# Kernel tuning notes

Measured on AMD Instinct MI355X. Metric: run time of the kernel, lower is better.

## Reference

```python
import jax, jax.numpy as jnp
import numpy as np

B, H, W, C = 16, 64, 64, 256
NH = 8          # num_heads
WS = 8          # window size (8,8) from shift=2
HID = 1024      # mlp hidden = 4*C
EPS = 1e-5


def _rel_index():
    # relative_position_index exactly as in the torch module (meshgrid 'ij')
    ch = np.arange(WS)
    coords = np.stack(np.meshgrid(ch, ch, indexing='ij'))          # (2, WS, WS)
    flat = coords.reshape(2, -1)                                    # (2, N)
    rel = flat[:, :, None] - flat[:, None, :]                       # (2, N, N)
    rel = rel.transpose(1, 2, 0).astype(np.int64)                   # (N, N, 2)
    rel[..., 0] += WS - 1
    rel[..., 1] += WS - 1
    rel[..., 0] *= 2 * WS - 1
    return jnp.asarray(rel.sum(-1))                                 # (N, N)


def _ln(x, w, b):
    m = x.mean(-1, keepdims=True)
    v = jnp.mean((x - m) ** 2, axis=-1, keepdims=True)
    return (x - m) / jnp.sqrt(v + EPS) * w + b


def setup_inputs() -> dict:
    key = jax.random.key(0)
    ks = jax.random.split(key, 16)
    std = 0.02
    n_bias = (2 * WS - 1) * (2 * WS - 1)  # 225
    return {
        'x': jax.random.normal(ks[0], (B, H * W, C), jnp.float32),
        'norm1_w': jnp.ones((C,), jnp.float32),
        'norm1_b': jnp.zeros((C,), jnp.float32),
        'qkv_w': jax.random.normal(ks[1], (3 * C, C), jnp.float32) * std,
        'qkv_b': jnp.zeros((3 * C,), jnp.float32),
        'rel_bias': jax.random.normal(ks[2], (n_bias, NH), jnp.float32) * std,
        'proj_w': jax.random.normal(ks[3], (C, C), jnp.float32) * std,
        'proj_b': jnp.zeros((C,), jnp.float32),
        'norm2_w': jnp.ones((C,), jnp.float32),
        'norm2_b': jnp.zeros((C,), jnp.float32),
        'fc1_w': jax.random.normal(ks[4], (HID, C), jnp.float32) * std,
        'fc1_b': jnp.zeros((HID,), jnp.float32),
        'dw_w': jax.random.normal(ks[5], (3, 3, 1, HID), jnp.float32) * std,  # HWIO depthwise
        'dw_b': jnp.zeros((HID,), jnp.float32),
        'fc2_w': jax.random.normal(ks[6], (C, HID), jnp.float32) * std,
        'fc2_b': jnp.zeros((C,), jnp.float32),
    }


def reference(x, norm1_w, norm1_b, qkv_w, qkv_b, rel_bias, proj_w, proj_b,
              norm2_w, norm2_b, fc1_w, fc1_b, dw_w, dw_b, fc2_w, fc2_b):
    S = (H // WS) * (W // WS)   # num windows = 64
    N = WS * WS                 # tokens per window = 64
    shortcut = x
    h = _ln(x, norm1_w, norm1_b).reshape(B, H, W, C)
    # window partition -> (B, S, N, C), then permute to (B, N, S, C)
    hw = (h.reshape(B, H // WS, WS, W // WS, WS, C)
            .transpose(0, 1, 3, 2, 4, 5)
            .reshape(B, S, N, C))
    xw = hw.transpose(0, 2, 1, 3)            # (B, N, S, C)
    # qkv over flattened (N*S) tokens; heads split the S*C feature dim
    xf = xw.reshape(B, N * S, C)
    qkv = xf @ qkv_w.T + qkv_b               # (B, N*S, 3C)
    qkv = qkv.reshape(B, N, 3, NH, S * C // NH).transpose(2, 0, 3, 1, 4)
    q, k, v = qkv[0], qkv[1], qkv[2]         # (B, NH, N, S*C/NH)
    scale = (C // NH) ** -0.5
    attn = jnp.einsum('bhnd,bhmd->bhnm', q, k) * scale   # (B, NH, N, N)
    idx = _rel_index()
    bias = rel_bias[idx.reshape(-1)].reshape(N, N, NH).transpose(2, 0, 1)
    attn = jax.nn.softmax(attn + bias[None], axis=-1)
    out = jnp.einsum('bhnm,bhmd->bhnd', attn, v)         # (B, NH, N, S*C/NH)
    out = out.transpose(0, 2, 1, 3).reshape(B, N * S, C)
    out = (out @ proj_w.T + proj_b).reshape(B, N, S, C).transpose(0, 2, 1, 3)  # (B,S,N,C)
    # window reverse -> (B, H*W, C)
    xr = (out.reshape(B, H // WS, W // WS, WS, WS, C)
             .transpose(0, 1, 3, 2, 4, 5)
             .reshape(B, H * W, C))
    x = shortcut + xr
    # conv-based MLP (eval mode, dropout = identity)
    y = _ln(x, norm2_w, norm2_b).reshape(B, H, H, C)      # NHWC
    y = jnp.einsum('bhwc,oc->bhwo', y, fc1_w) + fc1_b     # 1x1 conv
    y = jax.lax.conv_general_dilated(
        y, dw_w, (1, 1), 'SAME',
        dimension_numbers=('NHWC', 'HWIO', 'NHWC'),
        feature_group_count=HID) + dw_b
    y = jax.nn.gelu(y, approximate=False)
    y = jnp.einsum('bhwo,co->bhwc', y, fc2_w) + fc2_b     # 1x1 conv
    return x + y.reshape(B, H * W, C)
```

## Files before the change

kernel.cpp:

```cpp
#include <hip/hip_runtime.h>
#include <hip/hip_bf16.h>
#include <cstdint>
#include <cstddef>

#define B_     16
#define HW_    4096
#define C_     256
#define NH_    8
#define S_     64
#define N_     64
#define C3_    768
#define HID_   1024
#define DHEAD_ 2048
#define EPS_   1e-5f

using u16 = unsigned short;
using u32 = unsigned int;

typedef __attribute__((ext_vector_type(8))) short bf16x8;
typedef __attribute__((ext_vector_type(4))) float f32x4;

__device__ __forceinline__ float bf2f(u16 u) {
  union { float f; u32 i; } x; x.i = ((u32)u) << 16; return x.f;
}
__device__ __forceinline__ u16 f2bf(float f) {
  union { float f; u32 i; } x; x.f = f;
  u32 r = (x.i + 0x7FFFu + ((x.i >> 16) & 1u)) >> 16;
  return (u16)r;
}

__device__ __forceinline__ void gload_lds16(const u16* g, u16* l) {
  __builtin_amdgcn_global_load_lds(
      (const __attribute__((address_space(1))) unsigned int*)g,
      (__attribute__((address_space(3))) unsigned int*)l, 16, 0, 0);
}

__launch_bounds__(256)
__global__ void f2bf_kernel(const float* __restrict__ in, u16* __restrict__ out) {
  int i = blockIdx.x * 256 + threadIdx.x;
  float4 v = ((const float4*)in)[i];
  ushort4 o = {f2bf(v.x), f2bf(v.y), f2bf(v.z), f2bf(v.w)};
  ((ushort4*)out)[i] = o;
}

__launch_bounds__(256)
__global__ void ln_kernel(const float* __restrict__ in, const float* __restrict__ w,
                          const float* __restrict__ bias, u16* __restrict__ out,
                          int b_base) {
  int wave = threadIdx.x >> 6;
  int lane = threadIdx.x & 63;
  int t = blockIdx.x * 4 + wave;
  int b = b_base + (t >> 12);
  int r = t & 4095;
  int n = r >> 6, s = r & 63;
  int hw = (((s >> 3) << 3) + (n >> 3)) * 64 + ((s & 7) << 3) + (n & 7);
  size_t src_row = ((size_t)b << 12) + hw;
  float4 v = ((const float4*)(in + src_row * C_))[lane];
  float sum = v.x + v.y + v.z + v.w;
#pragma unroll
  for (int off = 32; off; off >>= 1) sum += __shfl_xor(sum, off);
  float mean = sum * (1.0f / C_);
  float4 d = {v.x - mean, v.y - mean, v.z - mean, v.w - mean};
  float ss = d.x * d.x + d.y * d.y + d.z * d.z + d.w * d.w;
#pragma unroll
  for (int off = 32; off; off >>= 1) ss += __shfl_xor(ss, off);
  float rstd = rsqrtf(ss * (1.0f / C_) + EPS_);
  float4 w4 = ((const float4*)w)[lane];
  float4 b4 = ((const float4*)bias)[lane];
  ushort4 o;
  o.x = f2bf(d.x * rstd * w4.x + b4.x);
  o.y = f2bf(d.y * rstd * w4.y + b4.y);
  o.z = f2bf(d.z * rstd * w4.z + b4.z);
  o.w = f2bf(d.w * rstd * w4.w + b4.w);
  ((ushort4*)(out + (size_t)t * C_))[lane] = o;
}

template<int K_, int J_, int EPI>
__launch_bounds__(256, 2)
__global__ void gemm_mfma(const u16* __restrict__ A, const u16* __restrict__ Wb,
                          const float* __restrict__ bias, u16* __restrict__ outB,
                          float* __restrict__ outF, const float* __restrict__ res,
                          int m_base, u16* __restrict__ qb, u16* __restrict__ kb,
                          u16* __restrict__ vt) {
  __shared__ u16 As[128 * 128];
  __shared__ u16 Bs[128 * 128];
  int tid = threadIdx.x;
  int wid = tid >> 6, lane = tid & 63;
  int n0 = blockIdx.x * 128;
  int m0 = blockIdx.y * 128;
  int wr = wid >> 1, wc = wid & 1;
  f32x4 acc[4][4] = {};

  int l16r = lane >> 4;
  int l16c = lane & 15;

  for (int k0 = 0; k0 < K_; k0 += 128) {
#pragma unroll
    for (int r = 0; r < 8; ++r) {
      int lrow = wid * 32 + r * 4 + l16r;
      int cb = (l16c * 16) ^ ((lrow & 7) << 4);
      gload_lds16(A + (size_t)(m0 + lrow) * K_ + k0 + (cb >> 1),
                  &As[(wid * 32 + r * 4) * 128]);
      gload_lds16(Wb + (size_t)(n0 + lrow) * K_ + k0 + (cb >> 1),
                  &Bs[(wid * 32 + r * 4) * 128]);
    }
    __syncthreads();
#pragma unroll
    for (int kk = 0; kk < 4; ++kk) {
      bf16x8 afr[4], bfr[4];
#pragma unroll
      for (int mf = 0; mf < 4; ++mf) {
        int ra = wr * 64 + mf * 16 + l16c;
        int cb = (kk * 64 + l16r * 16) ^ ((ra & 7) << 4);
        afr[mf] = *(const bf16x8*)&As[ra * 128 + (cb >> 1)];
      }
#pragma unroll
      for (int nf = 0; nf < 4; ++nf) {
        int rb = wc * 64 + nf * 16 + l16c;
        int cb = (kk * 64 + l16r * 16) ^ ((rb & 7) << 4);
        bfr[nf] = *(const bf16x8*)&Bs[rb * 128 + (cb >> 1)];
      }
#pragma unroll
      for (int mf = 0; mf < 4; ++mf)
#pragma unroll
        for (int nf = 0; nf < 4; ++nf)
          acc[mf][nf] = __builtin_amdgcn_mfma_f32_16x16x32_bf16(afr[mf], bfr[nf], acc[mf][nf], 0, 0, 0);
    }
    __syncthreads();
  }

#pragma unroll
  for (int nf = 0; nf < 4; ++nf) {
    int col = n0 + wc * 64 + nf * 16 + (lane & 15);
    float bv = bias[col];
#pragma unroll
    for (int mf = 0; mf < 4; ++mf) {
#pragma unroll
      for (int j = 0; j < 4; ++j) {
        int m = m0 + wr * 64 + mf * 16 + (lane >> 4) * 4 + j;
        float v = acc[mf][nf][j] + bv;
        if (EPI == 0) {
          outB[(size_t)m * J_ + col] = f2bf(v);
        } else if (EPI == 2) {
          size_t o = (size_t)(m_base + m) * C_ + col;
          outF[o] += v;
        } else {
          int b_rel = m >> 12, nn = (m >> 6) & 63, s = m & 63;
          int f = s * 768 + col;
          int part = f >> 14, hh = (f >> 11) & 7, d = f & 2047;
          u16 val = f2bf(v);
          size_t bh = (size_t)b_rel * 8 + hh;
          if (part == 0)      qb[(bh * 64 + nn) * 2048 + d] = val;
          else if (part == 1) kb[(bh * 64 + nn) * 2048 + d] = val;
          else                vt[(bh * 2048 + d) * 64 + nn] = val;
        }
      }
    }
  }
}

__launch_bounds__(256, 2)
__global__ void proj_ln_fused(const u16* __restrict__ A, const u16* __restrict__ Wb,
                              const float* __restrict__ bias, const float* __restrict__ res,
                              float* __restrict__ outF, const float* __restrict__ ln_w,
                              const float* __restrict__ ln_b, u16* __restrict__ h2,
                              int m_base) {
  __shared__ u16 As[64 * 128];
  __shared__ u16 Bs[256 * 128];
  __shared__ float red[64][8];
  int tid = threadIdx.x;
  int wid = tid >> 6, lane = tid & 63;
  int m0 = blockIdx.x * 64;
  f32x4 acc[4][4] = {};
  int l16r = lane >> 4, l16c = lane & 15;

  for (int k0 = 0; k0 < 256; k0 += 128) {
#pragma unroll
    for (int r = 0; r < 4; ++r) {
      int lrow = wid * 16 + r * 4 + l16r;
      int cb = (l16c * 16) ^ ((lrow & 7) << 4);
      gload_lds16(A + (size_t)(m0 + lrow) * 256 + k0 + (cb >> 1),
                  &As[(wid * 16 + r * 4) * 128]);
    }
#pragma unroll
    for (int r = 0; r < 16; ++r) {
      int lrow = wid * 64 + r * 4 + l16r;
      int cb = (l16c * 16) ^ ((lrow & 7) << 4);
      gload_lds16(Wb + (size_t)lrow * 256 + k0 + (cb >> 1),
                  &Bs[(wid * 64 + r * 4) * 128]);
    }
    __syncthreads();
#pragma unroll
    for (int kk = 0; kk < 4; ++kk) {
      bf16x8 afr[4], bfr[4];
#pragma unroll
      for (int mf = 0; mf < 4; ++mf) {
        int ra = mf * 16 + l16c;
        int cb = (kk * 64 + l16r * 16) ^ ((ra & 7) << 4);
        afr[mf] = *(const bf16x8*)&As[ra * 128 + (cb >> 1)];
      }
#pragma unroll
      for (int nf = 0; nf < 4; ++nf) {
        int rb = wid * 64 + nf * 16 + l16c;
        int cb = (kk * 64 + l16r * 16) ^ ((rb & 7) << 4);
        bfr[nf] = *(const bf16x8*)&Bs[rb * 128 + (cb >> 1)];
      }
#pragma unroll
      for (int mf = 0; mf < 4; ++mf)
#pragma unroll
        for (int nf = 0; nf < 4; ++nf)
          acc[mf][nf] = __builtin_amdgcn_mfma_f32_16x16x32_bf16(afr[mf], bfr[nf], acc[mf][nf], 0, 0, 0);
    }
    __syncthreads();
  }

#pragma unroll
  for (int mf = 0; mf < 4; ++mf) {
#pragma unroll
    for (int j = 0; j < 4; ++j) {
      int m = m0 + mf * 16 + (lane >> 4) * 4 + j;
      int gm = m_base + m;
      int b = gm >> 12, nn = (gm >> 6) & 63, s = gm & 63;
      int hw = (((s >> 3) << 3) + (nn >> 3)) * 64 + ((s & 7) << 3) + (nn & 7);
      size_t rowo = (((size_t)b << 12) + hw) * C_;
      float s1 = 0.f, s2 = 0.f;
#pragma unroll
      for (int nf = 0; nf < 4; ++nf) {
        int col = wid * 64 + nf * 16 + (lane & 15);
        float v = acc[mf][nf][j] + bias[col] + res[rowo + col];
        acc[mf][nf][j] = v;
        outF[rowo + col] = v;
        s1 += v; s2 += v * v;
      }
#pragma unroll
      for (int off = 1; off < 16; off <<= 1) {
        s1 += __shfl_xor(s1, off);
        s2 += __shfl_xor(s2, off);
      }
      if ((lane & 15) == 0) {
        int rr = mf * 16 + (lane >> 4) * 4 + j;
        red[rr][wid * 2] = s1;
        red[rr][wid * 2 + 1] = s2;
      }
    }
  }
  __syncthreads();

#pragma unroll
  for (int mf = 0; mf < 4; ++mf) {
#pragma unroll
    for (int j = 0; j < 4; ++j) {
      int rr = mf * 16 + (lane >> 4) * 4 + j;
      float sum = red[rr][0] + red[rr][2] + red[rr][4] + red[rr][6];
      float ssq = red[rr][1] + red[rr][3] + red[rr][5] + red[rr][7];
      float mean = sum * (1.0f / C_);
      float var = ssq * (1.0f / C_) - mean * mean;
      float rstd = rsqrtf(var + EPS_);
      int m = m0 + rr;
      int b_rel = m >> 12, nn = (m >> 6) & 63, s = m & 63;
      int hw = (((s >> 3) << 3) + (nn >> 3)) * 64 + ((s & 7) << 3) + (nn & 7);
      size_t ho = (((size_t)b_rel << 12) + hw) * C_;
#pragma unroll
      for (int nf = 0; nf < 4; ++nf) {
        int col = wid * 64 + nf * 16 + (lane & 15);
        float nv = (acc[mf][nf][j] - mean) * rstd * ln_w[col] + ln_b[col];
        h2[ho + col] = f2bf(nv);
      }
    }
  }
}

__launch_bounds__(256)
__global__ void attn_mfma(const u16* __restrict__ qb, const u16* __restrict__ kb,
                          const u16* __restrict__ vt, const float* __restrict__ rel_bias,
                          u16* __restrict__ outp) {
  __shared__ u16 bufA[4096];
  __shared__ u16 bufB[4096];
  int bh = blockIdx.x;
  int h = bh & 7;
  int b_rel = bh >> 3;
  int tid = threadIdx.x;
  int w = tid >> 6, lane = tid & 63;
  int l3 = lane >> 3, l7 = lane & 7;
  const u16* qg = qb + (size_t)bh * 64 * 2048;
  const u16* kg = kb + (size_t)bh * 64 * 2048;
  const u16* vg = vt + (size_t)bh * 2048 * 64;

  f32x4 acc[4] = {};
  for (int k0 = 0; k0 < 2048; k0 += 64) {
#pragma unroll
    for (int r = 0; r < 2; ++r) {
      int row = w * 16 + r * 8 + l3;
      int sc = (l7 ^ (row & 7)) * 8;
      gload_lds16(qg + (size_t)row * 2048 + k0 + sc, &bufA[(w * 16 + r * 8) * 64]);
      gload_lds16(kg + (size_t)row * 2048 + k0 + sc, &bufB[(w * 16 + r * 8) * 64]);
    }
    __syncthreads();
    int rowq = w * 16 + (lane & 15);
#pragma unroll
    for (int ks = 0; ks < 2; ++ks) {
      bf16x8 aq = *(const bf16x8*)&bufA[rowq * 64 + (((ks * 4 + (lane >> 4)) ^ (rowq & 7)) << 3)];
#pragma unroll
      for (int cf = 0; cf < 4; ++cf) {
        int m = cf * 16 + (lane & 15);
        bf16x8 bk = *(const bf16x8*)&bufB[m * 64 + (((ks * 4 + (lane >> 4)) ^ (m & 7)) << 3)];
        acc[cf] = __builtin_amdgcn_mfma_f32_16x16x32_bf16(aq, bk, acc[cf], 0, 0, 0);
      }
    }
    __syncthreads();
  }

  const float scale = 0.17677669529663688f;
#pragma unroll
  for (int j = 0; j < 4; ++j) {
    int r = w * 16 + (lane >> 4) * 4 + j;
    int i1 = r >> 3, j1 = r & 7;
    float v[4];
#pragma unroll
    for (int cf = 0; cf < 4; ++cf) {
      int c = cf * 16 + (lane & 15);
      int idx = (i1 - (c >> 3) + 7) * 15 + (j1 - (c & 7) + 7);
      v[cf] = acc[cf][j] * scale + rel_bias[idx * NH_ + h];
    }
    float mx = fmaxf(fmaxf(v[0], v[1]), fmaxf(v[2], v[3]));
#pragma unroll
    for (int off = 8; off; off >>= 1) mx = fmaxf(mx, __shfl_xor(mx, off));
    float sm = 0.f;
#pragma unroll
    for (int cf = 0; cf < 4; ++cf) { v[cf] = __expf(v[cf] - mx); sm += v[cf]; }
#pragma unroll
    for (int off = 8; off; off >>= 1) sm += __shfl_xor(sm, off);
    float inv = 1.0f / sm;
#pragma unroll
    for (int cf = 0; cf < 4; ++cf) {
      int c = cf * 16 + (lane & 15);
      bufA[r * 64 + (c ^ ((r & 7) << 3))] = f2bf(v[cf] * inv);
    }
  }
  __syncthreads();

  bf16x8 pa[2];
  {
    int n = w * 16 + (lane & 15);
#pragma unroll
    for (int ks = 0; ks < 2; ++ks)
      pa[ks] = *(const bf16x8*)&bufA[n * 64 + ((ks * 32 + (lane >> 4) * 8) ^ ((n & 7) << 3))];
  }

  for (int d0 = 0; d0 < 2048; d0 += 64) {
#pragma unroll
    for (int r = 0; r < 2; ++r) {
      int drow = w * 16 + r * 8 + l3;
      int sc = (l7 ^ (drow & 7)) * 8;
      gload_lds16(vg + (size_t)(d0 + drow) * 64 + sc, &bufB[(w * 16 + r * 8) * 64]);
    }
    __syncthreads();
    f32x4 o[4] = {};
#pragma unroll
    for (int ks = 0; ks < 2; ++ks)
#pragma unroll
      for (int cf = 0; cf < 4; ++cf) {
        int d = cf * 16 + (lane & 15);
        bf16x8 bv = *(const bf16x8*)&bufB[d * 64 + (((ks * 4 + (lane >> 4)) ^ (d & 7)) << 3)];
        o[cf] = __builtin_amdgcn_mfma_f32_16x16x32_bf16(pa[ks], bv, o[cf], 0, 0, 0);
      }
#pragma unroll
    for (int cf = 0; cf < 4; ++cf) {
      int f = h * 2048 + d0 + cf * 16 + (lane & 15);
      int s = f >> 8, c = f & 255;
#pragma unroll
      for (int j = 0; j < 4; ++j) {
        int n = w * 16 + (lane >> 4) * 4 + j;
        outp[(((size_t)b_rel * 64 + n) * 64 + s) * 256 + c] = f2bf(o[cf][j]);
      }
    }
    __syncthreads();
  }
}

__launch_bounds__(256)
__global__ void dwconv_gelu(const u16* __restrict__ y1, const float* __restrict__ dw_w,
                            const float* __restrict__ dw_b, u16* __restrict__ y2) {
  int bid = blockIdx.x;
  int wt = bid & 31, ht = (bid >> 5) & 15, b = bid >> 9;
  int h0 = ht * 4, w0 = wt * 2;
  int c0 = threadIdx.x * 4;

  float4 wv[9];
#pragma unroll
  for (int i = 0; i < 9; ++i) wv[i] = *(const float4*)&dw_w[i * HID_ + c0];

  ushort4 in[6][4];
#pragma unroll
  for (int ii = 0; ii < 6; ++ii) {
    int hh = h0 + ii - 1;
#pragma unroll
    for (int jj = 0; jj < 4; ++jj) {
      int ww = w0 + jj - 1;
      if ((unsigned)hh < 64u && (unsigned)ww < 64u)
        in[ii][jj] = *(const ushort4*)(y1 + ((size_t)((b << 12) + hh * 64 + ww)) * HID_ + c0);
      else
        in[ii][jj] = ushort4{0, 0, 0, 0};
    }
  }

  float4 bv = *(const float4*)&dw_b[c0];
  float4 acc[4][2];
#pragma unroll
  for (int i = 0; i < 4; ++i)
#pragma unroll
    for (int j = 0; j < 2; ++j) acc[i][j] = bv;

#pragma unroll
  for (int ii = 0; ii < 6; ++ii) {
#pragma unroll
    for (int jj = 0; jj < 4; ++jj) {
      ushort4 u = in[ii][jj];
      float4 f = {bf2f(u.x), bf2f(u.y), bf2f(u.z), bf2f(u.w)};
#pragma unroll
      for (int kh = 0; kh < 3; ++kh) {
        int i = ii - kh;
        if (i < 0 || i > 3) continue;
#pragma unroll
        for (int kw = 0; kw < 3; ++kw) {
          int j = jj - kw;
          if (j < 0 || j > 1) continue;
          float4 w4 = wv[kh * 3 + kw];
          acc[i][j].x += f.x * w4.x;
          acc[i][j].y += f.y * w4.y;
          acc[i][j].z += f.z * w4.z;
          acc[i][j].w += f.w * w4.w;
        }
      }
    }
  }

  const float k = 0.70710678118654752f;
#pragma unroll
  for (int i = 0; i < 4; ++i) {
#pragma unroll
    for (int j = 0; j < 2; ++j) {
      float4 a = acc[i][j];
      ushort4 o;
      o.x = f2bf(0.5f * a.x * (1.0f + erff(a.x * k)));
      o.y = f2bf(0.5f * a.y * (1.0f + erff(a.y * k)));
      o.z = f2bf(0.5f * a.z * (1.0f + erff(a.z * k)));
      o.w = f2bf(0.5f * a.w * (1.0f + erff(a.w * k)));
      *(ushort4*)(y2 + ((size_t)((b << 12) + (h0 + i) * 64 + (w0 + j))) * HID_ + c0) = o;
    }
  }
}

extern "C" void kernel_launch(void* const* d_in, const int* in_sizes, int n_in,
                              void* d_out, int out_size, void* d_ws, size_t ws_size,
                              hipStream_t stream) {
  const float* x       = (const float*)d_in[0];
  const float* norm1_w = (const float*)d_in[1];
  const float* norm1_b = (const float*)d_in[2];
  const float* qkv_w   = (const float*)d_in[3];
  const float* qkv_b   = (const float*)d_in[4];
  const float* rel_b   = (const float*)d_in[5];
  const float* proj_w  = (const float*)d_in[6];
  const float* proj_b  = (const float*)d_in[7];
  const float* norm2_w = (const float*)d_in[8];
  const float* norm2_b = (const float*)d_in[9];
  const float* fc1_w   = (const float*)d_in[10];
  const float* fc1_b   = (const float*)d_in[11];
  const float* dw_w    = (const float*)d_in[12];
  const float* dw_b    = (const float*)d_in[13];
  const float* fc2_w   = (const float*)d_in[14];
  const float* fc2_b   = (const float*)d_in[15];
  float* out = (float*)d_out;
  char* ws = (char*)d_ws;

  u16* wq = (u16*)(ws);
  u16* wp = wq + 768 * 256;
  u16* w1 = wp + 256 * 256;
  u16* w2 = w1 + 1024 * 256;
  f2bf_kernel<<<768 * 256 / 1024, 256, 0, stream>>>(qkv_w, wq);
  f2bf_kernel<<<256 * 256 / 1024, 256, 0, stream>>>(proj_w, wp);
  f2bf_kernel<<<1024 * 256 / 1024, 256, 0, stream>>>(fc1_w, w1);
  f2bf_kernel<<<1024 * 256 / 1024, 256, 0, stream>>>(fc2_w, w2);

  const size_t MBy = (size_t)1 << 20;
  char* cws = ws + 2 * MBy;
  int G = 1;
  for (int g = 16; g >= 1; g >>= 1) {
    if (2 * MBy + (size_t)(18 * g) * MBy <= ws_size) { G = g; break; }
  }
  const size_t gm = (size_t)G * MBy;
  u16* h1c    = (u16*)(cws);
  u16* qbuf   = (u16*)(cws + 2 * gm);
  u16* kbuf   = (u16*)(cws + 4 * gm);
  u16* vtbuf  = (u16*)(cws + 6 * gm);
  u16* attnoc = (u16*)(cws + 8 * gm);
  u16* h2c    = (u16*)(cws);
  u16* y1c    = (u16*)(cws + 2 * gm);
  u16* y2c    = (u16*)(cws + 10 * gm);

  const int Mloc = G * 4096;
  for (int b0 = 0; b0 < B_; b0 += G) {
    ln_kernel<<<Mloc / 4, 256, 0, stream>>>(x, norm1_w, norm1_b, h1c, b0);
    gemm_mfma<256, 768, 3><<<dim3(6, Mloc / 128), 256, 0, stream>>>(
        h1c, wq, qkv_b, nullptr, nullptr, nullptr, 0, qbuf, kbuf, vtbuf);
    attn_mfma<<<G * 8, 256, 0, stream>>>(qbuf, kbuf, vtbuf, rel_b, attnoc);
    proj_ln_fused<<<Mloc / 64, 256, 0, stream>>>(
        attnoc, wp, proj_b, x, out, norm2_w, norm2_b, h2c, b0 * 4096);
    gemm_mfma<256, 1024, 0><<<dim3(8, Mloc / 128), 256, 0, stream>>>(
        h2c, w1, fc1_b, y1c, nullptr, nullptr, 0, nullptr, nullptr, nullptr);
    dwconv_gelu<<<Mloc / 8, 256, 0, stream>>>(y1c, dw_w, dw_b, y2c);
    gemm_mfma<1024, 256, 2><<<dim3(2, Mloc / 128), 256, 0, stream>>>(
        y2c, w2, fc2_b, nullptr, out, nullptr, b0 * 4096, nullptr, nullptr, nullptr);
  }
}
```

Before: 547.1 us.

## Double-buffer LDS tiles with BK=64 in gemm and proj_ln kernels

Both MFMA GEMM kernels switch from a single 128-wide K tile to two 64-wide K buffers. The next tile is prefetched with direct-to-LDS loads while the current one is computed, and a single waitcnt plus barrier sits at the end of each step. This hides global load latency behind MFMA work. The proj_ln kernel also reuses the A buffer for its reduction scratch, freeing LDS. The risks are the extra barriers per K step and the correctness of the new XOR swizzle and the buffer aliasing.

```diff
diff --git a/kernel.cpp b/kernel.cpp
--- a/kernel.cpp
+++ b/kernel.cpp
@@ -82,8 +82,9 @@
                           float* __restrict__ outF, const float* __restrict__ res,
                           int m_base, u16* __restrict__ qb, u16* __restrict__ kb,
                           u16* __restrict__ vt) {
-  __shared__ u16 As[128 * 128];
-  __shared__ u16 Bs[128 * 128];
+  constexpr int NT = K_ / 64;
+  __shared__ u16 As[2][128 * 64];
+  __shared__ u16 Bs[2][128 * 64];
   int tid = threadIdx.x;
   int wid = tid >> 6, lane = tid & 63;
   int n0 = blockIdx.x * 128;
@@ -91,34 +92,48 @@
   int wr = wid >> 1, wc = wid & 1;
   f32x4 acc[4][4] = {};
 
-  int l16r = lane >> 4;
-  int l16c = lane & 15;
-
-  for (int k0 = 0; k0 < K_; k0 += 128) {
-#pragma unroll
-    for (int r = 0; r < 8; ++r) {
-      int lrow = wid * 32 + r * 4 + l16r;
-      int cb = (l16c * 16) ^ ((lrow & 7) << 4);
-      gload_lds16(A + (size_t)(m0 + lrow) * K_ + k0 + (cb >> 1),
-                  &As[(wid * 32 + r * 4) * 128]);
-      gload_lds16(Wb + (size_t)(n0 + lrow) * K_ + k0 + (cb >> 1),
-                  &Bs[(wid * 32 + r * 4) * 128]);
-    }
-    __syncthreads();
-#pragma unroll
-    for (int kk = 0; kk < 4; ++kk) {
+  int srow8 = lane >> 3;
+  int sslot = lane & 7;
+
+#define GSTAGE(buf, t)                                                         \
+  {                                                                            \
+    int k0g = (t) * 64;                                                        \
+    _Pragma("unroll")                                                          \
+    for (int r = 0; r < 4; ++r) {                                              \
+      int row = wid * 32 + r * 8 + srow8;                                      \
+      int cb = ((sslot ^ srow8) << 4);                                         \
+      gload_lds16(A + (size_t)(m0 + row) * K_ + k0g + (cb >> 1),               \
+                  &As[buf][(wid * 32 + r * 8) * 64]);                          \
+      gload_lds16(Wb + (size_t)(n0 + row) * K_ + k0g + (cb >> 1),              \
+                  &Bs[buf][(wid * 32 + r * 8) * 64]);                          \
+    }                                                                          \
+  }
+
+  GSTAGE(0, 0);
+  asm volatile("s_waitcnt vmcnt(0)" ::: "memory");
+  __builtin_amdgcn_sched_barrier(0);
+  __builtin_amdgcn_s_barrier();
+  __builtin_amdgcn_sched_barrier(0);
+
+#pragma unroll
+  for (int t = 0; t < NT; ++t) {
+    if (t + 1 < NT) GSTAGE((t + 1) & 1, t + 1);
+    const u16* as = As[t & 1];
+    const u16* bs = Bs[t & 1];
+#pragma unroll
+    for (int kk = 0; kk < 2; ++kk) {
       bf16x8 afr[4], bfr[4];
 #pragma unroll
       for (int mf = 0; mf < 4; ++mf) {
-        int ra = wr * 64 + mf * 16 + l16c;
-        int cb = (kk * 64 + l16r * 16) ^ ((ra & 7) << 4);
-        afr[mf] = *(const bf16x8*)&As[ra * 128 + (cb >> 1)];
+        int ra = wr * 64 + mf * 16 + (lane & 15);
+        int cb = (((kk * 4 + (lane >> 4)) ^ (ra & 7)) << 4);
+        afr[mf] = *(const bf16x8*)&as[ra * 64 + (cb >> 1)];
       }
 #pragma unroll
       for (int nf = 0; nf < 4; ++nf) {
-        int rb = wc * 64 + nf * 16 + l16c;
-        int cb = (kk * 64 + l16r * 16) ^ ((rb & 7) << 4);
-        bfr[nf] = *(const bf16x8*)&Bs[rb * 128 + (cb >> 1)];
+        int rb = wc * 64 + nf * 16 + (lane & 15);
+        int cb = (((kk * 4 + (lane >> 4)) ^ (rb & 7)) << 4);
+        bfr[nf] = *(const bf16x8*)&bs[rb * 64 + (cb >> 1)];
       }
 #pragma unroll
       for (int mf = 0; mf < 4; ++mf)
@@ -126,8 +141,12 @@
         for (int nf = 0; nf < 4; ++nf)
           acc[mf][nf] = __builtin_amdgcn_mfma_f32_16x16x32_bf16(afr[mf], bfr[nf], acc[mf][nf], 0, 0, 0);
     }
-    __syncthreads();
-  }
+    asm volatile("s_waitcnt vmcnt(0)" ::: "memory");
+    __builtin_amdgcn_sched_barrier(0);
+    __builtin_amdgcn_s_barrier();
+    __builtin_amdgcn_sched_barrier(0);
+  }
+#undef GSTAGE
 
 #pragma unroll
   for (int nf = 0; nf < 4; ++nf) {
@@ -165,45 +184,57 @@
                               float* __restrict__ outF, const float* __restrict__ ln_w,
                               const float* __restrict__ ln_b, u16* __restrict__ h2,
                               int m_base) {
-  __shared__ u16 As[64 * 128];
-  __shared__ u16 Bs[256 * 128];
-  __shared__ float red[64][8];
+  __shared__ u16 As[2][64 * 64];
+  __shared__ u16 Bs[2][256 * 64];
   int tid = threadIdx.x;
   int wid = tid >> 6, lane = tid & 63;
   int m0 = blockIdx.x * 64;
   f32x4 acc[4][4] = {};
-  int l16r = lane >> 4, l16c = lane & 15;
-
-  for (int k0 = 0; k0 < 256; k0 += 128) {
-#pragma unroll
-    for (int r = 0; r < 4; ++r) {
-      int lrow = wid * 16 + r * 4 + l16r;
-      int cb = (l16c * 16) ^ ((lrow & 7) << 4);
-      gload_lds16(A + (size_t)(m0 + lrow) * 256 + k0 + (cb >> 1),
-                  &As[(wid * 16 + r * 4) * 128]);
-    }
-#pragma unroll
-    for (int r = 0; r < 16; ++r) {
-      int lrow = wid * 64 + r * 4 + l16r;
-      int cb = (l16c * 16) ^ ((lrow & 7) << 4);
-      gload_lds16(Wb + (size_t)lrow * 256 + k0 + (cb >> 1),
-                  &Bs[(wid * 64 + r * 4) * 128]);
-    }
-    __syncthreads();
-#pragma unroll
-    for (int kk = 0; kk < 4; ++kk) {
+  int srow8 = lane >> 3, sslot = lane & 7;
+
+#define PSTAGE(buf, t)                                                         \
+  {                                                                            \
+    int k0g = (t) * 64;                                                        \
+    int cb = ((sslot ^ srow8) << 4);                                           \
+    _Pragma("unroll")                                                          \
+    for (int r = 0; r < 2; ++r) {                                              \
+      int row = wid * 16 + r * 8 + srow8;                                      \
+      gload_lds16(A + (size_t)(m0 + row) * 256 + k0g + (cb >> 1),              \
+                  &As[buf][(wid * 16 + r * 8) * 64]);                          \
+    }                                                                          \
+    _Pragma("unroll")                                                          \
+    for (int r = 0; r < 8; ++r) {                                              \
+      int row = wid * 64 + r * 8 + srow8;                                      \
+      gload_lds16(Wb + (size_t)row * 256 + k0g + (cb >> 1),                    \
+                  &Bs[buf][(wid * 64 + r * 8) * 64]);                          \
+    }                                                                          \
+  }
+
+  PSTAGE(0, 0);
+  asm volatile("s_waitcnt vmcnt(0)" ::: "memory");
+  __builtin_amdgcn_sched_barrier(0);
+  __builtin_amdgcn_s_barrier();
+  __builtin_amdgcn_sched_barrier(0);
+
+#pragma unroll
+  for (int t = 0; t < 4; ++t) {
+    if (t + 1 < 4) PSTAGE((t + 1) & 1, t + 1);
+    const u16* as = As[t & 1];
+    const u16* bs = Bs[t & 1];
+#pragma unroll
+    for (int kk = 0; kk < 2; ++kk) {
       bf16x8 afr[4], bfr[4];
 #pragma unroll
       for (int mf = 0; mf < 4; ++mf) {
-        int ra = mf * 16 + l16c;
-        int cb = (kk * 64 + l16r * 16) ^ ((ra & 7) << 4);
-        afr[mf] = *(const bf16x8*)&As[ra * 128 + (cb >> 1)];
+        int ra = mf * 16 + (lane & 15);
+        int cb = (((kk * 4 + (lane >> 4)) ^ (ra & 7)) << 4);
+        afr[mf] = *(const bf16x8*)&as[ra * 64 + (cb >> 1)];
       }
 #pragma unroll
       for (int nf = 0; nf < 4; ++nf) {
-        int rb = wid * 64 + nf * 16 + l16c;
-        int cb = (kk * 64 + l16r * 16) ^ ((rb & 7) << 4);
-        bfr[nf] = *(const bf16x8*)&Bs[rb * 128 + (cb >> 1)];
+        int rb = wid * 64 + nf * 16 + (lane & 15);
+        int cb = (((kk * 4 + (lane >> 4)) ^ (rb & 7)) << 4);
+        bfr[nf] = *(const bf16x8*)&bs[rb * 64 + (cb >> 1)];
       }
 #pragma unroll
       for (int mf = 0; mf < 4; ++mf)
@@ -211,8 +242,14 @@
         for (int nf = 0; nf < 4; ++nf)
           acc[mf][nf] = __builtin_amdgcn_mfma_f32_16x16x32_bf16(afr[mf], bfr[nf], acc[mf][nf], 0, 0, 0);
     }
-    __syncthreads();
-  }
+    asm volatile("s_waitcnt vmcnt(0)" ::: "memory");
+    __builtin_amdgcn_sched_barrier(0);
+    __builtin_amdgcn_s_barrier();
+    __builtin_amdgcn_sched_barrier(0);
+  }
+#undef PSTAGE
+
+  float (*red)[8] = (float (*)[8])As;
 
 #pragma unroll
   for (int mf = 0; mf < 4; ++mf) {
```

Measured after the change: 541.6 us. No clear change (-1.0%).
